# Optimization experiments

Hardware: AMD Instinct MI355X
Metric: run time of the kernel (lower is better)

The kernel has to match this reference:

```python
import jax, jax.numpy as jnp
import numpy as np

B, T, H, D = 4, 2048, 16, 64
HID = H * D
ROPE_THETA = 10000.0


def _rope_tables(t, d, theta):
    # frequencies over half the head dim, duplicated to full head_dim
    inv_freq = 1.0 / (theta ** (np.arange(0, d, 2, dtype=np.float32) / d))  # (d/2,)
    pos = np.arange(t, dtype=np.float32)
    freqs = np.outer(pos, inv_freq)                      # (T, d/2)
    emb = np.concatenate([freqs, freqs], axis=-1)        # (T, d)
    return jnp.asarray(np.cos(emb)), jnp.asarray(np.sin(emb))


def setup_inputs() -> dict:
    key = jax.random.key(0)
    ks = jax.random.split(key, 5)
    s = 1.0 / np.sqrt(HID)
    cos, sin = _rope_tables(T, D, ROPE_THETA)
    return {
        "x": jax.random.normal(ks[0], (B, T, HID), dtype=jnp.float32),
        "cos": cos,
        "sin": sin,
        "wq": jax.random.normal(ks[1], (HID, HID), dtype=jnp.float32) * s,
        "wk": jax.random.normal(ks[2], (HID, HID), dtype=jnp.float32) * s,
        "wv": jax.random.normal(ks[3], (HID, HID), dtype=jnp.float32) * s,
        "wo": jax.random.normal(ks[4], (HID, HID), dtype=jnp.float32) * s,
    }


def _rotate_half(x):
    x1, x2 = jnp.split(x, 2, axis=-1)
    return jnp.concatenate([-x2, x1], axis=-1)


def reference(x, cos, sin, wq, wk, wv, wo):
    b, t, _ = x.shape
    # QKV projections (nn.Linear: y = x @ W^T), reshape to (B, H, T, D)
    q = (x @ wq.T).reshape(b, t, H, D).transpose(0, 2, 1, 3)
    k = (x @ wk.T).reshape(b, t, H, D).transpose(0, 2, 1, 3)
    v = (x @ wv.T).reshape(b, t, H, D).transpose(0, 2, 1, 3)
    # RoPE
    c = cos[None, None, :, :]
    s = sin[None, None, :, :]
    q = q * c + _rotate_half(q) * s
    k = k * c + _rotate_half(k) * s
    # causal SDPA
    scale = 1.0 / jnp.sqrt(jnp.asarray(D, dtype=x.dtype))
    scores = jnp.einsum("bhqd,bhkd->bhqk", q, k) * scale
    causal = jnp.tril(jnp.ones((t, t), dtype=bool))
    scores = jnp.where(causal[None, None], scores, jnp.finfo(scores.dtype).min)
    attn = jax.nn.softmax(scores, axis=-1)
    out = jnp.einsum("bhqk,bhkd->bhqd", attn, v)
    out = out.transpose(0, 2, 1, 3).reshape(b, t, HID)
    return out @ wo.T
```

## Files before the change

kernel.cpp:

```cpp
#include <hip/hip_runtime.h>

#define BSZ 4
#define TT 2048
#define NH 16
#define HD 64
#define HID 1024
#define BT 8192
#define BH 64

typedef unsigned short u16;
typedef unsigned int u32;
typedef unsigned long long u64;
typedef __attribute__((ext_vector_type(4))) float f32x4;
typedef __attribute__((ext_vector_type(8))) short bf16x8;

#define MFMA32(a, b, c) __builtin_amdgcn_mfma_f32_16x16x32_bf16(a, b, c, 0, 0, 0)

typedef const __attribute__((address_space(1))) u32* gp32;
typedef __attribute__((address_space(3))) u32* lp32;

__device__ __forceinline__ u16 f2bf(float f) {
    union { float f; u32 u; } x; x.f = f;
    u32 r = x.u + 0x7FFFu + ((x.u >> 16) & 1u);
    return (u16)(r >> 16);
}

__device__ __forceinline__ float fexp2(float x) {
    float r;
    asm("v_exp_f32 %0, %1\n\ts_nop 1" : "=v"(r) : "v"(x));
    return r;
}

__global__ __launch_bounds__(256) void cast_kernel(const float* __restrict__ src,
                                                   u16* __restrict__ dst, int n4) {
    int i = blockIdx.x * 256 + threadIdx.x;
    if (i >= n4) return;
    f32x4 v = *(const f32x4*)(src + (size_t)i * 4);
    uint2 u;
    u.x = (u32)f2bf(v[0]) | ((u32)f2bf(v[1]) << 16);
    u.y = (u32)f2bf(v[2]) | ((u32)f2bf(v[3]) << 16);
    *(uint2*)(dst + (size_t)i * 4) = u;
}

__global__ __launch_bounds__(256)
void cast_w_kernel(const float* __restrict__ wq, const float* __restrict__ wk,
                   const float* __restrict__ wv, const float* __restrict__ wo,
                   u16* __restrict__ wqkv, u16* __restrict__ wo_bf) {
    int g = blockIdx.x >> 10;
    int i = (blockIdx.x & 1023) * 256 + threadIdx.x;
    const float* src = (g == 0) ? wq : (g == 1) ? wk : (g == 2) ? wv : wo;
    u16* dst = (g == 3) ? wo_bf : wqkv + (size_t)g * HID * HID;
    f32x4 v = *(const f32x4*)(src + (size_t)i * 4);
    uint2 u;
    u.x = (u32)f2bf(v[0]) | ((u32)f2bf(v[1]) << 16);
    u.y = (u32)f2bf(v[2]) | ((u32)f2bf(v[3]) << 16);
    *(uint2*)(dst + (size_t)i * 4) = u;
}

template<int MODE>
__global__ __launch_bounds__(512, 2)
void gemm_bt(const u16* __restrict__ A, const u16* __restrict__ W,
             float* __restrict__ Cf, u16* __restrict__ qkv, u16* __restrict__ vt,
             const float* __restrict__ cosT, const float* __restrict__ sinT) {
    __shared__ __align__(16) u16 sh[3 * 24576];
    const int tid  = threadIdx.x;
    const int wid  = tid >> 6, lane = tid & 63;
    const int lrow = lane & 15, lk = lane >> 4;
    const int wm   = (wid >> 1) * 64, wn = (wid & 1) * 64;
    const int xcd  = blockIdx.x & 7;
    const int i_   = blockIdx.x >> 3;
    const int mt   = xcd * 4 + (i_ & 3);
    const int nt   = i_ >> 2;
    const int m0   = mt * 256, n0 = nt * 128;

    auto stageA = [&](int buf, int kk, int half) {
        u16* dst = sh + buf * 24576;
        #pragma unroll
        for (int s = 0; s < 2; ++s) {
            int l16 = half * 1024 + s * 512 + tid;
            int r = l16 >> 3, c = l16 & 7;
            int gc = (c ^ (r & 7)) * 8;
            __builtin_amdgcn_global_load_lds(
                (gp32)&A[(size_t)(m0 + r) * HID + kk + gc],
                (lp32)&dst[l16 * 8], 16, 0, 0);
        }
    };
    auto stageB = [&](int buf, int kk) {
        u16* dst = sh + buf * 24576 + 16384;
        #pragma unroll
        for (int s = 0; s < 2; ++s) {
            int l16 = s * 512 + tid;
            int r = l16 >> 3, c = l16 & 7;
            int gc = (c ^ (r & 7)) * 8;
            __builtin_amdgcn_global_load_lds(
                (gp32)&W[(size_t)(n0 + r) * HID + kk + gc],
                (lp32)&dst[l16 * 8], 16, 0, 0);
        }
    };

    f32x4 acc[4][4] = {};

    stageA(0, 0, 0); stageA(0, 0, 1); stageB(0, 0);
    stageA(1, 64, 0); stageA(1, 64, 1); stageB(1, 64);

    int b = 0;
    for (int t = 0; t < 16; ++t) {
        if (t < 15) asm volatile("s_waitcnt vmcnt(6)" ::: "memory");
        else        asm volatile("s_waitcnt vmcnt(0)" ::: "memory");
        __builtin_amdgcn_s_barrier();
        const u16* As = sh + b * 24576;
        const u16* Bs = As + 16384;
        int b2 = b + 2; if (b2 >= 3) b2 -= 3;

        bf16x8 af[2][4], bfr[2][4];
        #pragma unroll
        for (int h = 0; h < 2; ++h) {
            #pragma unroll
            for (int i = 0; i < 4; ++i) {
                int row = wm + i * 16 + lrow;
                int pc  = (h * 4 + lk) ^ (row & 7);
                af[h][i] = *(const bf16x8*)&As[row * 64 + pc * 8];
            }
            #pragma unroll
            for (int j = 0; j < 4; ++j) {
                int row = wn + j * 16 + lrow;
                int pc  = (h * 4 + lk) ^ (row & 7);
                bfr[h][j] = *(const bf16x8*)&Bs[row * 64 + pc * 8];
            }
        }
        if (t + 2 < 16) {
            const int kk2 = (t + 2) * 64;
            stageA(b2, kk2, 0); stageB(b2, kk2); stageA(b2, kk2, 1);
        }
        __builtin_amdgcn_s_setprio(1);
        #pragma unroll
        for (int h = 0; h < 2; ++h)
            #pragma unroll
            for (int i = 0; i < 4; ++i)
                #pragma unroll
                for (int j = 0; j < 4; ++j)
                    acc[i][j] = MFMA32(af[h][i], bfr[h][j], acc[i][j]);
        __builtin_amdgcn_s_setprio(0);
        ++b; if (b == 3) b = 0;
    }
    __syncthreads();

    if (MODE == 0) {
        const int bb = m0 >> 11, tl0 = m0 & (TT - 1);
        if (nt < 16) {
            const float QSC = (nt < 8) ? 0.125f * 1.44269504f : 1.0f;
            #pragma unroll
            for (int i = 0; i < 4; ++i)
                #pragma unroll
                for (int r = 0; r < 4; ++r) {
                    int tl = (m0 + wm + i * 16 + lk * 4 + r) & (TT - 1);
                    #pragma unroll
                    for (int j = 0; j < 2; ++j) {
                        int dd = j * 16 + lrow;
                        float c = cosT[tl * HD + dd], s = sinT[tl * HD + dd];
                        float v1 = acc[i][j][r], v2 = acc[i][j + 2][r];
                        acc[i][j][r]     = (v1 * c - v2 * s) * QSC;
                        acc[i][j + 2][r] = (v2 * c + v1 * s) * QSC;
                    }
                }
            #pragma unroll
            for (int i = 0; i < 4; ++i)
                #pragma unroll
                for (int j = 0; j < 4; ++j)
                    #pragma unroll
                    for (int r = 0; r < 4; ++r)
                        sh[(wm + i * 16 + lk * 4 + r) * 136 + wn + j * 16 + lrow] =
                            f2bf(acc[i][j][r]);
            __syncthreads();
            #pragma unroll
            for (int p = 0; p < 8; ++p) {
                int idx = p * 512 + tid;
                int r = idx >> 4, c16 = idx & 15;
                f32x4 v = *(const f32x4*)&sh[r * 136 + c16 * 8];
                int nfull = n0 + c16 * 8;
                int proj = nfull >> 10, nl = nfull & 1023;
                int h = nl >> 6, d = nl & 63;
                u16* dst = qkv + (size_t)proj * BT * HID +
                           (((size_t)(bb * NH + h) * TT + tl0 + r) * HD + d);
                *(f32x4*)dst = v;
            }
        } else {
            #pragma unroll
            for (int i = 0; i < 4; ++i)
                #pragma unroll
                for (int j = 0; j < 4; ++j)
                    #pragma unroll
                    for (int r = 0; r < 4; ++r)
                        sh[(wn + j * 16 + lrow) * 272 + wm + i * 16 + lk * 4 + r] =
                            f2bf(acc[i][j][r]);
            __syncthreads();
            #pragma unroll
            for (int p = 0; p < 8; ++p) {
                int oc  = p * 512 + tid;
                int t8  = oc & 31;
                int col = oc >> 5;
                f32x4 v = *(const f32x4*)&sh[col * 272 + t8 * 8];
                int nl = (n0 - 2048) + col;
                int h = nl >> 6, d = nl & 63;
                *(f32x4*)&vt[((size_t)(bb * NH + h) * HD + d) * TT + tl0 + t8 * 8] = v;
            }
        }
    } else {
        #pragma unroll
        for (int i = 0; i < 4; ++i)
            #pragma unroll
            for (int j = 0; j < 4; ++j)
                #pragma unroll
                for (int r = 0; r < 4; ++r) {
                    int m = m0 + wm + i * 16 + lk * 4 + r;
                    int n = n0 + wn + j * 16 + lrow;
                    Cf[(size_t)m * HID + n] = acc[i][j][r];
                }
    }
}

__device__ __forceinline__ u32 cvtpk(float lo, float hi) {
    u32 r;
    asm("v_cvt_pk_bf16_f32 %0, %1, %2" : "=v"(r) : "v"(lo), "v"(hi));
    return r;
}
__device__ __forceinline__ bf16x8 packP(const f32x4& a, const f32x4& b) {
    union { bf16x8 v; u32 w[4]; } u;
    u.w[0] = cvtpk(a[0], a[1]); u.w[1] = cvtpk(a[2], a[3]);
    u.w[2] = cvtpk(b[0], b[1]); u.w[3] = cvtpk(b[2], b[3]);
    return u.v;
}

#define VST 68

__global__ __launch_bounds__(256)
void attn_kernel(const u16* __restrict__ q, const u16* __restrict__ k,
                 const u16* __restrict__ vt, u16* __restrict__ o) {
    __shared__ u16 Ks[64 * 72];
    __shared__ u16 Vts[64 * VST];
    const int tid  = threadIdx.x;
    const int w    = tid >> 6, lane = tid & 63;
    const int lrow = lane & 15, lk = lane >> 4;
    const int nlid = (blockIdx.x & 7) * 128 + (blockIdx.x >> 3);
    const int p    = nlid & 15;
    const int bh   = nlid >> 4;
    const int q0a  = 64 * p, q0b = 64 * (31 - p);
    const size_t hb = (size_t)bh * TT * HD;

    bf16x8 qfa[2], qfb[2];
    #pragma unroll
    for (int kq = 0; kq < 2; ++kq) {
        qfa[kq] = *(const bf16x8*)&q[hb + (size_t)(q0a + w * 16 + lrow) * HD + kq * 32 + lk * 8];
        qfb[kq] = *(const bf16x8*)&q[hb + (size_t)(q0b + w * 16 + lrow) * HD + kq * 32 + lk * 8];
    }

    f32x4 oa[4] = {}, obc[4] = {};
    f32x4 la4 = {}, lb4 = {};

    const int r0 = tid >> 3, f0 = (tid & 7) * 8;
    const int r1 = (tid + 256) >> 3, f1 = (tid & 7) * 8;

    f32x4 pk0 = *(const f32x4*)&k[hb + (size_t)r0 * HD + f0];
    f32x4 pk1 = *(const f32x4*)&k[hb + (size_t)r1 * HD + f1];
    f32x4 pv0 = *(const f32x4*)&vt[hb + (size_t)r0 * TT + f0];
    f32x4 pv1 = *(const f32x4*)&vt[hb + (size_t)r1 * TT + f1];

    const int nIter = 32 - p;
    for (int it = 0; it < nIter; ++it) {
        const bool a_act = (it <= p);
        __syncthreads();
        *(f32x4*)&Ks[r0 * 72 + f0]   = pk0;
        *(f32x4*)&Ks[r1 * 72 + f1]   = pk1;
        *(f32x4*)&Vts[r0 * VST + f0] = pv0;
        *(f32x4*)&Vts[r1 * VST + f1] = pv1;
        __syncthreads();
        if (it + 1 < nIter) {
            const int nn = (it + 1) * 64;
            pk0 = *(const f32x4*)&k[hb + (size_t)(nn + r0) * HD + f0];
            pk1 = *(const f32x4*)&k[hb + (size_t)(nn + r1) * HD + f1];
            pv0 = *(const f32x4*)&vt[hb + (size_t)r0 * TT + nn + f0];
            pv1 = *(const f32x4*)&vt[hb + (size_t)r1 * TT + nn + f1];
        }

        bf16x8 kf0[4], kf1[4];
        #pragma unroll
        for (int mt = 0; mt < 4; ++mt) {
            kf0[mt] = *(const bf16x8*)&Ks[(mt * 16 + lrow) * 72 + lk * 8];
            kf1[mt] = *(const bf16x8*)&Ks[(mt * 16 + lrow) * 72 + 32 + lk * 8];
        }

        {
            f32x4 s[4] = {};
            __builtin_amdgcn_s_setprio(1);
            #pragma unroll
            for (int mt = 0; mt < 4; ++mt) {
                s[mt] = MFMA32(kf0[mt], qfb[0], s[mt]);
                s[mt] = MFMA32(kf1[mt], qfb[1], s[mt]);
            }
            __builtin_amdgcn_s_setprio(0);
            if (it == nIter - 1) {
                #pragma unroll
                for (int mt = 0; mt < 4; ++mt)
                    #pragma unroll
                    for (int r = 0; r < 4; ++r)
                        if (mt * 16 + lk * 4 + r > w * 16 + lrow) s[mt][r] = -1e30f;
            }
            #pragma unroll
            for (int mt = 0; mt < 4; ++mt) {
                #pragma unroll
                for (int r = 0; r < 4; ++r) s[mt][r] = fexp2(s[mt][r]);
                lb4 += s[mt];
            }
            bf16x8 p0 = packP(s[0], s[1]), p1 = packP(s[2], s[3]);
            __builtin_amdgcn_s_setprio(1);
            #pragma unroll
            for (int t2 = 0; t2 < 2; ++t2)
                #pragma unroll
                for (int dm = 0; dm < 4; ++dm) {
                    union { bf16x8 v; struct { u64 lo, hi; } u; } vf;
                    const u16* vrow = &Vts[(dm * 16 + lrow) * VST + t2 * 32 + lk * 4];
                    vf.u.lo = *(const u64*)vrow;
                    vf.u.hi = *(const u64*)(vrow + 16);
                    obc[dm] = MFMA32(vf.v, t2 ? p1 : p0, obc[dm]);
                }
            __builtin_amdgcn_s_setprio(0);
        }

        if (a_act) {
            f32x4 s[4] = {};
            __builtin_amdgcn_s_setprio(1);
            #pragma unroll
            for (int mt = 0; mt < 4; ++mt) {
                s[mt] = MFMA32(kf0[mt], qfa[0], s[mt]);
                s[mt] = MFMA32(kf1[mt], qfa[1], s[mt]);
            }
            __builtin_amdgcn_s_setprio(0);
            if (it == p) {
                #pragma unroll
                for (int mt = 0; mt < 4; ++mt)
                    #pragma unroll
                    for (int r = 0; r < 4; ++r)
                        if (mt * 16 + lk * 4 + r > w * 16 + lrow) s[mt][r] = -1e30f;
            }
            #pragma unroll
            for (int mt = 0; mt < 4; ++mt) {
                #pragma unroll
                for (int r = 0; r < 4; ++r) s[mt][r] = fexp2(s[mt][r]);
                la4 += s[mt];
            }
            bf16x8 p0 = packP(s[0], s[1]), p1 = packP(s[2], s[3]);
            __builtin_amdgcn_s_setprio(1);
            #pragma unroll
            for (int t2 = 0; t2 < 2; ++t2)
                #pragma unroll
                for (int dm = 0; dm < 4; ++dm) {
                    union { bf16x8 v; struct { u64 lo, hi; } u; } vf;
                    const u16* vrow = &Vts[(dm * 16 + lrow) * VST + t2 * 32 + lk * 4];
                    vf.u.lo = *(const u64*)vrow;
                    vf.u.hi = *(const u64*)(vrow + 16);
                    oa[dm] = MFMA32(vf.v, t2 ? p1 : p0, oa[dm]);
                }
            __builtin_amdgcn_s_setprio(0);
        }
    }

    float lia = la4[0] + la4[1] + la4[2] + la4[3];
    float lib = lb4[0] + lb4[1] + lb4[2] + lb4[3];
    lia += __shfl_xor(lia, 16, 64); lia += __shfl_xor(lia, 32, 64);
    lib += __shfl_xor(lib, 16, 64); lib += __shfl_xor(lib, 32, 64);
    const int b = bh >> 4, h = bh & 15;
    const float inva = 1.f / lia, invb = 1.f / lib;
    #pragma unroll
    for (int dm = 0; dm < 4; ++dm) {
        uint2 pk;
        pk.x = cvtpk(oa[dm][0] * inva, oa[dm][1] * inva);
        pk.y = cvtpk(oa[dm][2] * inva, oa[dm][3] * inva);
        int row = q0a + w * 16 + lrow;
        *(uint2*)&o[((size_t)(b * TT + row)) * HID + h * HD + dm * 16 + lk * 4] = pk;
        pk.x = cvtpk(obc[dm][0] * invb, obc[dm][1] * invb);
        pk.y = cvtpk(obc[dm][2] * invb, obc[dm][3] * invb);
        row = q0b + w * 16 + lrow;
        *(uint2*)&o[((size_t)(b * TT + row)) * HID + h * HD + dm * 16 + lk * 4] = pk;
    }
}

extern "C" void kernel_launch(void* const* d_in, const int* in_sizes, int n_in,
                              void* d_out, int out_size, void* d_ws, size_t ws_size,
                              hipStream_t stream) {
    const float* x    = (const float*)d_in[0];
    const float* cosT = (const float*)d_in[1];
    const float* sinT = (const float*)d_in[2];
    const float* wq   = (const float*)d_in[3];
    const float* wk   = (const float*)d_in[4];
    const float* wv   = (const float*)d_in[5];
    const float* wo   = (const float*)d_in[6];
    float* out = (float*)d_out;

    char* ws = (char*)d_ws;
    size_t off = 0;
    u16* x_bf  = (u16*)(ws + off); off += (size_t)BT * HID * 2;
    u16* wqkv  = (u16*)(ws + off); off += (size_t)3 * HID * HID * 2;
    u16* wo_bf = (u16*)(ws + off); off += (size_t)HID * HID * 2;
    u16* qb    = (u16*)(ws + off); off += (size_t)BT * HID * 2;
    u16* kb    = (u16*)(ws + off); off += (size_t)BT * HID * 2;
    u16* vtb   = (u16*)(ws + off); off += (size_t)BT * HID * 2;
    u16* ob    = (u16*)(ws + off); off += (size_t)BT * HID * 2;
    (void)kb;

    cast_kernel<<<(BT * HID / 4 + 255) / 256, 256, 0, stream>>>(x, x_bf, BT * HID / 4);
    cast_w_kernel<<<4096, 256, 0, stream>>>(wq, wk, wv, wo, wqkv, wo_bf);

    gemm_bt<0><<<dim3(768), 512, 0, stream>>>(
        x_bf, wqkv, nullptr, qb, vtb, cosT, sinT);

    attn_kernel<<<dim3(1024), 256, 0, stream>>>(qb, kb, vtb, ob);

    gemm_bt<1><<<dim3(256), 512, 0, stream>>>(
        ob, wo_bf, out, nullptr, nullptr, nullptr, nullptr);
}
```

Measured before the change: 239.1 us.

## Split paired causal query tiles into one tile per block with longest-first order

The attention kernel previously paired a short and a long query tile per block so that all blocks did balanced work. It now gives each block a single 64-row query tile, launches twice as many blocks, and orders them so the longest tiles are scheduled first. It also asks for 5 blocks per CU through launch bounds and batches four exp instructions behind one s_nop. The intent is more parallelism and lower register pressure. In exchange, K/V tiles are staged once per query tile instead of being shared by two, which roughly doubles K/V global and LDS traffic.

```diff
diff --git a/kernel.cpp b/kernel.cpp
--- a/kernel.cpp
+++ b/kernel.cpp
@@ -25,10 +25,15 @@
     return (u16)(r >> 16);
 }
 
-__device__ __forceinline__ float fexp2(float x) {
-    float r;
-    asm("v_exp_f32 %0, %1\n\ts_nop 1" : "=v"(r) : "v"(x));
-    return r;
+__device__ __forceinline__ void fexp2x4(f32x4& v) {
+    float a = v[0], b = v[1], c = v[2], d = v[3];
+    asm("v_exp_f32 %0, %0\n\t"
+        "v_exp_f32 %1, %1\n\t"
+        "v_exp_f32 %2, %2\n\t"
+        "v_exp_f32 %3, %3\n\t"
+        "s_nop 1"
+        : "+v"(a), "+v"(b), "+v"(c), "+v"(d));
+    v[0] = a; v[1] = b; v[2] = c; v[3] = d;
 }
 
 __global__ __launch_bounds__(256) void cast_kernel(const float* __restrict__ src,
@@ -233,7 +238,7 @@
 
 #define VST 68
 
-__global__ __launch_bounds__(256)
+__global__ __launch_bounds__(256, 5)
 void attn_kernel(const u16* __restrict__ q, const u16* __restrict__ k,
                  const u16* __restrict__ vt, u16* __restrict__ o) {
     __shared__ u16 Ks[64 * 72];
@@ -241,21 +246,19 @@
     const int tid  = threadIdx.x;
     const int w    = tid >> 6, lane = tid & 63;
     const int lrow = lane & 15, lk = lane >> 4;
-    const int nlid = (blockIdx.x & 7) * 128 + (blockIdx.x >> 3);
-    const int p    = nlid & 15;
-    const int bh   = nlid >> 4;
-    const int q0a  = 64 * p, q0b = 64 * (31 - p);
+    const int nlid = (blockIdx.x & 7) * 256 + (blockIdx.x >> 3);
+    const int qt   = 31 - (nlid & 31);
+    const int bh   = nlid >> 5;
+    const int q0   = 64 * qt;
     const size_t hb = (size_t)bh * TT * HD;
 
-    bf16x8 qfa[2], qfb[2];
+    bf16x8 qf[2];
     #pragma unroll
-    for (int kq = 0; kq < 2; ++kq) {
-        qfa[kq] = *(const bf16x8*)&q[hb + (size_t)(q0a + w * 16 + lrow) * HD + kq * 32 + lk * 8];
-        qfb[kq] = *(const bf16x8*)&q[hb + (size_t)(q0b + w * 16 + lrow) * HD + kq * 32 + lk * 8];
-    }
-
-    f32x4 oa[4] = {}, obc[4] = {};
-    f32x4 la4 = {}, lb4 = {};
+    for (int kq = 0; kq < 2; ++kq)
+        qf[kq] = *(const bf16x8*)&q[hb + (size_t)(q0 + w * 16 + lrow) * HD + kq * 32 + lk * 8];
+
+    f32x4 o4[4] = {};
+    f32x4 l4 = {};
 
     const int r0 = tid >> 3, f0 = (tid & 7) * 8;
     const int r1 = (tid + 256) >> 3, f1 = (tid & 7) * 8;
@@ -265,9 +268,8 @@
     f32x4 pv0 = *(const f32x4*)&vt[hb + (size_t)r0 * TT + f0];
     f32x4 pv1 = *(const f32x4*)&vt[hb + (size_t)r1 * TT + f1];
 
-    const int nIter = 32 - p;
+    const int nIter = qt + 1;
     for (int it = 0; it < nIter; ++it) {
-        const bool a_act = (it <= p);
         __syncthreads();
         *(f32x4*)&Ks[r0 * 72 + f0]   = pk0;
         *(f32x4*)&Ks[r1 * 72 + f1]   = pk1;
@@ -279,7 +281,7 @@
             pk0 = *(const f32x4*)&k[hb + (size_t)(nn + r0) * HD + f0];
             pk1 = *(const f32x4*)&k[hb + (size_t)(nn + r1) * HD + f1];
             pv0 = *(const f32x4*)&vt[hb + (size_t)r0 * TT + nn + f0];
-            pv1 = *(const f32x4*)&vt[hb + (size_t)r1 * TT + nn + f1];
+            pv1 = *(const f32x4*)&vt[hb + (size_t)r0 * TT + nn + f1 + (r1 - r0) * TT - (f1 - f0)];
         }
 
         bf16x8 kf0[4], kf1[4];
@@ -289,97 +291,51 @@
             kf1[mt] = *(const bf16x8*)&Ks[(mt * 16 + lrow) * 72 + 32 + lk * 8];
         }
 
-        {
-            f32x4 s[4] = {};
-            __builtin_amdgcn_s_setprio(1);
-            #pragma unroll
-            for (int mt = 0; mt < 4; ++mt) {
-                s[mt] = MFMA32(kf0[mt], qfb[0], s[mt]);
-                s[mt] = MFMA32(kf1[mt], qfb[1], s[mt]);
-            }
-            __builtin_amdgcn_s_setprio(0);
-            if (it == nIter - 1) {
-                #pragma unroll
-                for (int mt = 0; mt < 4; ++mt)
-                    #pragma unroll
-                    for (int r = 0; r < 4; ++r)
-                        if (mt * 16 + lk * 4 + r > w * 16 + lrow) s[mt][r] = -1e30f;
-            }
-            #pragma unroll
-            for (int mt = 0; mt < 4; ++mt) {
-                #pragma unroll
-                for (int r = 0; r < 4; ++r) s[mt][r] = fexp2(s[mt][r]);
-                lb4 += s[mt];
-            }
-            bf16x8 p0 = packP(s[0], s[1]), p1 = packP(s[2], s[3]);
-            __builtin_amdgcn_s_setprio(1);
-            #pragma unroll
-            for (int t2 = 0; t2 < 2; ++t2)
-                #pragma unroll
-                for (int dm = 0; dm < 4; ++dm) {
-                    union { bf16x8 v; struct { u64 lo, hi; } u; } vf;
-                    const u16* vrow = &Vts[(dm * 16 + lrow) * VST + t2 * 32 + lk * 4];
-                    vf.u.lo = *(const u64*)vrow;
-                    vf.u.hi = *(const u64*)(vrow + 16);
-                    obc[dm] = MFMA32(vf.v, t2 ? p1 : p0, obc[dm]);
-                }
-            __builtin_amdgcn_s_setprio(0);
-        }
-
-        if (a_act) {
-            f32x4 s[4] = {};
-            __builtin_amdgcn_s_setprio(1);
-            #pragma unroll
-            for (int mt = 0; mt < 4; ++mt) {
-                s[mt] = MFMA32(kf0[mt], qfa[0], s[mt]);
-                s[mt] = MFMA32(kf1[mt], qfa[1], s[mt]);
-            }
-            __builtin_amdgcn_s_setprio(0);
-            if (it == p) {
-                #pragma unroll
-                for (int mt = 0; mt < 4; ++mt)
-                    #pragma unroll
-                    for (int r = 0; r < 4; ++r)
-                        if (mt * 16 + lk * 4 + r > w * 16 + lrow) s[mt][r] = -1e30f;
-            }
-            #pragma unroll
-            for (int mt = 0; mt < 4; ++mt) {
-                #pragma unroll
-                for (int r = 0; r < 4; ++r) s[mt][r] = fexp2(s[mt][r]);
-                la4 += s[mt];
-            }
-            bf16x8 p0 = packP(s[0], s[1]), p1 = packP(s[2], s[3]);
-            __builtin_amdgcn_s_setprio(1);
-            #pragma unroll
-            for (int t2 = 0; t2 < 2; ++t2)
-                #pragma unroll
-                for (int dm = 0; dm < 4; ++dm) {
-                    union { bf16x8 v; struct { u64 lo, hi; } u; } vf;
-                    const u16* vrow = &Vts[(dm * 16 + lrow) * VST + t2 * 32 + lk * 4];
-                    vf.u.lo = *(const u64*)vrow;
-                    vf.u.hi = *(const u64*)(vrow + 16);
-                    oa[dm] = MFMA32(vf.v, t2 ? p1 : p0, oa[dm]);
-                }
-            __builtin_amdgcn_s_setprio(0);
-        }
+        f32x4 s[4] = {};
+        __builtin_amdgcn_s_setprio(1);
+        #pragma unroll
+        for (int mt = 0; mt < 4; ++mt) {
+            s[mt] = MFMA32(kf0[mt], qf[0], s[mt]);
+            s[mt] = MFMA32(kf1[mt], qf[1], s[mt]);
+        }
+        __builtin_amdgcn_s_setprio(0);
+        if (it == nIter - 1) {
+            #pragma unroll
+            for (int mt = 0; mt < 4; ++mt)
+                #pragma unroll
+                for (int r = 0; r < 4; ++r)
+                    if (mt * 16 + lk * 4 + r > w * 16 + lrow) s[mt][r] = -1e30f;
+        }
+        #pragma unroll
+        for (int mt = 0; mt < 4; ++mt) {
+            fexp2x4(s[mt]);
+            l4 += s[mt];
+        }
+        bf16x8 p0 = packP(s[0], s[1]), p1 = packP(s[2], s[3]);
+        __builtin_amdgcn_s_setprio(1);
+        #pragma unroll
+        for (int t2 = 0; t2 < 2; ++t2)
+            #pragma unroll
+            for (int dm = 0; dm < 4; ++dm) {
+                union { bf16x8 v; struct { u64 lo, hi; } u; } vf;
+                const u16* vrow = &Vts[(dm * 16 + lrow) * VST + t2 * 32 + lk * 4];
+                vf.u.lo = *(const u64*)vrow;
+                vf.u.hi = *(const u64*)(vrow + 16);
+                o4[dm] = MFMA32(vf.v, t2 ? p1 : p0, o4[dm]);
+            }
+        __builtin_amdgcn_s_setprio(0);
     }
 
-    float lia = la4[0] + la4[1] + la4[2] + la4[3];
-    float lib = lb4[0] + lb4[1] + lb4[2] + lb4[3];
-    lia += __shfl_xor(lia, 16, 64); lia += __shfl_xor(lia, 32, 64);
-    lib += __shfl_xor(lib, 16, 64); lib += __shfl_xor(lib, 32, 64);
+    float li = l4[0] + l4[1] + l4[2] + l4[3];
+    li += __shfl_xor(li, 16, 64); li += __shfl_xor(li, 32, 64);
     const int b = bh >> 4, h = bh & 15;
-    const float inva = 1.f / lia, invb = 1.f / lib;
+    const float inv = 1.f / li;
+    const int row = q0 + w * 16 + lrow;
     #pragma unroll
     for (int dm = 0; dm < 4; ++dm) {
         uint2 pk;
-        pk.x = cvtpk(oa[dm][0] * inva, oa[dm][1] * inva);
-        pk.y = cvtpk(oa[dm][2] * inva, oa[dm][3] * inva);
-        int row = q0a + w * 16 + lrow;
-        *(uint2*)&o[((size_t)(b * TT + row)) * HID + h * HD + dm * 16 + lk * 4] = pk;
-        pk.x = cvtpk(obc[dm][0] * invb, obc[dm][1] * invb);
-        pk.y = cvtpk(obc[dm][2] * invb, obc[dm][3] * invb);
-        row = q0b + w * 16 + lrow;
+        pk.x = cvtpk(o4[dm][0] * inv, o4[dm][1] * inv);
+        pk.y = cvtpk(o4[dm][2] * inv, o4[dm][3] * inv);
         *(uint2*)&o[((size_t)(b * TT + row)) * HID + h * HD + dm * 16 + lk * 4] = pk;
     }
 }
@@ -413,7 +369,7 @@
     gemm_bt<0><<<dim3(768), 512, 0, stream>>>(
         x_bf, wqkv, nullptr, qb, vtb, cosT, sinT);
 
-    attn_kernel<<<dim3(1024), 256, 0, stream>>>(qb, kb, vtb, ob);
+    attn_kernel<<<dim3(2048), 256, 0, stream>>>(qb, kb, vtb, ob);
 
     gemm_bt<1><<<dim3(256), 512, 0, stream>>>(
         ob, wo_bf, out, nullptr, nullptr, nullptr, nullptr);
```

Result: slower. 265.3 us (+11.0%).

## Split K fragment loads, batch QK MFMAs for both tiles, batch exp asm

Applied to the files above, without the earlier changes.

Loads K fragments in two halves and issues the QK^T MFMAs for both query tiles back to back, so only half the K fragments are live at once and the MFMA pipe gets a longer run. It also emits four v_exp_f32 per asm block with one s_nop instead of one nop per exp, and adds sched_barriers plus a min-waves hint in launch_bounds to cap register use for higher occupancy. The risks are that keeping both score accumulators live raises register pressure, and that the fixed schedule barriers limit how the compiler can interleave work.

```diff
diff --git a/kernel.cpp b/kernel.cpp
--- a/kernel.cpp
+++ b/kernel.cpp
@@ -25,10 +25,15 @@
     return (u16)(r >> 16);
 }
 
-__device__ __forceinline__ float fexp2(float x) {
-    float r;
-    asm("v_exp_f32 %0, %1\n\ts_nop 1" : "=v"(r) : "v"(x));
-    return r;
+__device__ __forceinline__ void fexp2x4(f32x4& v) {
+    float a = v[0], b = v[1], c = v[2], d = v[3];
+    asm("v_exp_f32 %0, %0\n\t"
+        "v_exp_f32 %1, %1\n\t"
+        "v_exp_f32 %2, %2\n\t"
+        "v_exp_f32 %3, %3\n\t"
+        "s_nop 1"
+        : "+v"(a), "+v"(b), "+v"(c), "+v"(d));
+    v[0] = a; v[1] = b; v[2] = c; v[3] = d;
 }
 
 __global__ __launch_bounds__(256) void cast_kernel(const float* __restrict__ src,
@@ -233,7 +238,7 @@
 
 #define VST 68
 
-__global__ __launch_bounds__(256)
+__global__ __launch_bounds__(256, 4)
 void attn_kernel(const u16* __restrict__ q, const u16* __restrict__ k,
                  const u16* __restrict__ vt, u16* __restrict__ o) {
     __shared__ u16 Ks[64 * 72];
@@ -282,36 +287,51 @@
             pv1 = *(const f32x4*)&vt[hb + (size_t)r1 * TT + nn + f1];
         }
 
-        bf16x8 kf0[4], kf1[4];
+        f32x4 sb[4] = {}, sa[4] = {};
+        {
+            bf16x8 kf[4];
+            #pragma unroll
+            for (int mt = 0; mt < 4; ++mt)
+                kf[mt] = *(const bf16x8*)&Ks[(mt * 16 + lrow) * 72 + lk * 8];
+            __builtin_amdgcn_s_setprio(1);
+            #pragma unroll
+            for (int mt = 0; mt < 4; ++mt) sb[mt] = MFMA32(kf[mt], qfb[0], sb[mt]);
+            if (a_act) {
+                #pragma unroll
+                for (int mt = 0; mt < 4; ++mt) sa[mt] = MFMA32(kf[mt], qfa[0], sa[mt]);
+            }
+            __builtin_amdgcn_s_setprio(0);
+        }
+        {
+            bf16x8 kf[4];
+            #pragma unroll
+            for (int mt = 0; mt < 4; ++mt)
+                kf[mt] = *(const bf16x8*)&Ks[(mt * 16 + lrow) * 72 + 32 + lk * 8];
+            __builtin_amdgcn_s_setprio(1);
+            #pragma unroll
+            for (int mt = 0; mt < 4; ++mt) sb[mt] = MFMA32(kf[mt], qfb[1], sb[mt]);
+            if (a_act) {
+                #pragma unroll
+                for (int mt = 0; mt < 4; ++mt) sa[mt] = MFMA32(kf[mt], qfa[1], sa[mt]);
+            }
+            __builtin_amdgcn_s_setprio(0);
+        }
+        __builtin_amdgcn_sched_barrier(0);
+
+        if (it == nIter - 1) {
+            #pragma unroll
+            for (int mt = 0; mt < 4; ++mt)
+                #pragma unroll
+                for (int r = 0; r < 4; ++r)
+                    if (mt * 16 + lk * 4 + r > w * 16 + lrow) sb[mt][r] = -1e30f;
+        }
         #pragma unroll
         for (int mt = 0; mt < 4; ++mt) {
-            kf0[mt] = *(const bf16x8*)&Ks[(mt * 16 + lrow) * 72 + lk * 8];
-            kf1[mt] = *(const bf16x8*)&Ks[(mt * 16 + lrow) * 72 + 32 + lk * 8];
-        }
-
+            fexp2x4(sb[mt]);
+            lb4 += sb[mt];
+        }
         {
-            f32x4 s[4] = {};
-            __builtin_amdgcn_s_setprio(1);
-            #pragma unroll
-            for (int mt = 0; mt < 4; ++mt) {
-                s[mt] = MFMA32(kf0[mt], qfb[0], s[mt]);
-                s[mt] = MFMA32(kf1[mt], qfb[1], s[mt]);
-            }
-            __builtin_amdgcn_s_setprio(0);
-            if (it == nIter - 1) {
-                #pragma unroll
-                for (int mt = 0; mt < 4; ++mt)
-                    #pragma unroll
-                    for (int r = 0; r < 4; ++r)
-                        if (mt * 16 + lk * 4 + r > w * 16 + lrow) s[mt][r] = -1e30f;
-            }
-            #pragma unroll
-            for (int mt = 0; mt < 4; ++mt) {
-                #pragma unroll
-                for (int r = 0; r < 4; ++r) s[mt][r] = fexp2(s[mt][r]);
-                lb4 += s[mt];
-            }
-            bf16x8 p0 = packP(s[0], s[1]), p1 = packP(s[2], s[3]);
+            bf16x8 p0 = packP(sb[0], sb[1]), p1 = packP(sb[2], sb[3]);
             __builtin_amdgcn_s_setprio(1);
             #pragma unroll
             for (int t2 = 0; t2 < 2; ++t2)
@@ -325,30 +345,22 @@
                 }
             __builtin_amdgcn_s_setprio(0);
         }
+        __builtin_amdgcn_sched_barrier(0);
 
         if (a_act) {
-            f32x4 s[4] = {};
-            __builtin_amdgcn_s_setprio(1);
-            #pragma unroll
-            for (int mt = 0; mt < 4; ++mt) {
-                s[mt] = MFMA32(kf0[mt], qfa[0], s[mt]);
-                s[mt] = MFMA32(kf1[mt], qfa[1], s[mt]);
-            }
-            __builtin_amdgcn_s_setprio(0);
             if (it == p) {
                 #pragma unroll
                 for (int mt = 0; mt < 4; ++mt)
                     #pragma unroll
                     for (int r = 0; r < 4; ++r)
-                        if (mt * 16 + lk * 4 + r > w * 16 + lrow) s[mt][r] = -1e30f;
+                        if (mt * 16 + lk * 4 + r > w * 16 + lrow) sa[mt][r] = -1e30f;
             }
             #pragma unroll
             for (int mt = 0; mt < 4; ++mt) {
-                #pragma unroll
-                for (int r = 0; r < 4; ++r) s[mt][r] = fexp2(s[mt][r]);
-                la4 += s[mt];
-            }
-            bf16x8 p0 = packP(s[0], s[1]), p1 = packP(s[2], s[3]);
+                fexp2x4(sa[mt]);
+                la4 += sa[mt];
+            }
+            bf16x8 p0 = packP(sa[0], sa[1]), p1 = packP(sa[2], sa[3]);
             __builtin_amdgcn_s_setprio(1);
             #pragma unroll
             for (int t2 = 0; t2 < 2; ++t2)
```

Result: slower. 324.2 us (+35.6%).
